# Performance work log

Hardware: AMD Instinct MI355X
Metric: run time of the kernel (lower is better)

The kernel has to match this reference:

```python
import jax, jax.numpy as jnp
import numpy as np

B, S, DIM = 1, 2048, 2048
H = 16
Q_LORA, KV_LORA = 1536, 512
D_NOPE, D_ROPE, D_V = 128, 64, 128
D_QK = D_NOPE + D_ROPE  # 192
EPS = 1e-6


def rms_norm(x, w, eps=EPS):
    var = jnp.mean(jnp.square(x), axis=-1, keepdims=True)
    return x * jax.lax.rsqrt(var + eps) * w


def apply_rope(x, cos, sin):
    # x: [B,S,H,D] with interleaved complex pairs; cos/sin: [S,D//2]
    x1, x2 = x[..., 0::2], x[..., 1::2]
    c = cos[None, :, None, :]
    s = sin[None, :, None, :]
    o1 = x1 * c - x2 * s
    o2 = x1 * s + x2 * c
    return jnp.stack([o1, o2], axis=-1).reshape(x.shape)


def setup_inputs() -> dict:
    key = jax.random.key(0)
    ks = jax.random.split(key, 8)
    x = jax.random.normal(ks[0], (B, S, DIM), dtype=jnp.float32)
    # rotary tables (standard complex exponentials)
    inv_freq = 1.0 / (10000.0 ** (np.arange(0, D_ROPE, 2, dtype=np.float32) / D_ROPE))
    t = np.arange(S, dtype=np.float32)
    freqs = np.outer(t, inv_freq)  # [S, D_ROPE//2]
    freqs_cos = jnp.asarray(np.cos(freqs))
    freqs_sin = jnp.asarray(np.sin(freqs))
    sd = lambda fan_in: 1.0 / np.sqrt(fan_in)
    wq_a = jax.random.normal(ks[1], (Q_LORA, DIM), dtype=jnp.float32) * sd(DIM)
    q_a_ln_w = jnp.ones((Q_LORA,), dtype=jnp.float32)
    wq_b = jax.random.normal(ks[2], (H * D_QK, Q_LORA), dtype=jnp.float32) * sd(Q_LORA)
    wkv_a = jax.random.normal(ks[3], (KV_LORA + D_ROPE, DIM), dtype=jnp.float32) * sd(DIM)
    kv_a_ln_w = jnp.ones((KV_LORA,), dtype=jnp.float32)
    wkv_b = jax.random.normal(ks[4], (H * (D_NOPE + D_V), KV_LORA), dtype=jnp.float32) * sd(KV_LORA)
    wo = jax.random.normal(ks[5], (DIM, H * D_V), dtype=jnp.float32) * sd(H * D_V)
    return {"x": x, "freqs_cos": freqs_cos, "freqs_sin": freqs_sin,
            "wq_a": wq_a, "q_a_ln_w": q_a_ln_w, "wq_b": wq_b,
            "wkv_a": wkv_a, "kv_a_ln_w": kv_a_ln_w, "wkv_b": wkv_b, "wo": wo}


def reference(x, freqs_cos, freqs_sin, wq_a, q_a_ln_w, wq_b, wkv_a, kv_a_ln_w, wkv_b, wo):
    softmax_scale = D_QK ** -0.5
    # Query: low-rank down-proj -> RMSNorm -> up-proj
    q = rms_norm(x @ wq_a.T, q_a_ln_w) @ wq_b.T            # [B,S,H*D_QK]
    q = q.reshape(B, S, H, D_QK)
    q_nope, q_pe = q[..., :D_NOPE], q[..., D_NOPE:]
    q_pe = apply_rope(q_pe, freqs_cos, freqs_sin)
    # KV: shared low-rank latent + decoupled rope key (MQA-style, 1 head)
    kv = x @ wkv_a.T                                        # [B,S,KV_LORA+D_ROPE]
    kv_c = rms_norm(kv[..., :KV_LORA], kv_a_ln_w)           # [B,S,KV_LORA]
    k_pe = apply_rope(kv[..., None, KV_LORA:], freqs_cos, freqs_sin)  # [B,S,1,D_ROPE]
    kvb = (kv_c @ wkv_b.T).reshape(B, S, H, D_NOPE + D_V)
    k_nope, v = kvb[..., :D_NOPE], kvb[..., D_NOPE:]
    # Attention scores: nope part + shared rope part
    scores = (jnp.einsum('bqhd,bkhd->bhqk', q_nope, k_nope)
              + jnp.einsum('bqhd,bkd->bhqk', q_pe, k_pe[:, :, 0, :])) * softmax_scale
    causal = jnp.tril(jnp.ones((S, S), dtype=bool))
    scores = jnp.where(causal[None, None], scores, -jnp.inf)
    p = jax.nn.softmax(scores, axis=-1)
    out = jnp.einsum('bhqk,bkhd->bqhd', p, v).reshape(B, S, H * D_V)
    return out @ wo.T
```

## Files before the change

kernel.cpp:

```cpp
#include <hip/hip_runtime.h>
#include <cstdint>
#include <cstddef>

typedef __bf16 bf16;
typedef bf16 bf16x8 __attribute__((ext_vector_type(8)));
typedef bf16 bf16x4 __attribute__((ext_vector_type(4)));
typedef float f32x4 __attribute__((ext_vector_type(4)));

typedef __attribute__((address_space(1))) void as1_void;
typedef __attribute__((address_space(3))) void as3_void;

#define INF __builtin_inff()

__global__ __launch_bounds__(256) void z100_cast_all(
    const float* __restrict__ x, const float* __restrict__ wq_a,
    const float* __restrict__ wkv_a, const float* __restrict__ wq_b,
    const float* __restrict__ wkv_b, const float* __restrict__ wo,
    bf16* __restrict__ x_bf, bf16* __restrict__ wab_bf,
    bf16* __restrict__ wqb_bf, bf16* __restrict__ wkvb_bf,
    bf16* __restrict__ wo_bf) {
    int i = blockIdx.x * 256 + threadIdx.x;
    const float* s;
    bf16* d;
    if (i < 1048576)      { s = x + (size_t)i * 4;                     d = x_bf + (size_t)i * 4; }
    else if (i < 1835008) { int o = i - 1048576; s = wq_a  + (size_t)o * 4; d = wab_bf + (size_t)o * 4; }
    else if (i < 2129920) { int o = i - 1835008; s = wkv_a + (size_t)o * 4; d = wab_bf + 1536ull * 2048 + (size_t)o * 4; }
    else if (i < 3309568) { int o = i - 2129920; s = wq_b  + (size_t)o * 4; d = wqb_bf + (size_t)o * 4; }
    else if (i < 3833856) { int o = i - 3309568; s = wkv_b + (size_t)o * 4; d = wkvb_bf + (size_t)o * 4; }
    else if (i < 4882432) { int o = i - 3833856; s = wo    + (size_t)o * 4; d = wo_bf + (size_t)o * 4; }
    else {                  int o = i - 4882432; bf16x4 z = {};
                            *(bf16x4*)(wab_bf + 2112ull * 2048 + (size_t)o * 4) = z; return; }
    float4 v = *(const float4*)s;
    bf16x4 ovec = { (bf16)v.x, (bf16)v.y, (bf16)v.z, (bf16)v.w };
    *(bf16x4*)d = ovec;
}

__global__ __launch_bounds__(256) void z100_rmsnorm(
    const float* __restrict__ x, int ldx, const float* __restrict__ w,
    bf16* __restrict__ y, int N, float invN) {
    const int row = blockIdx.x;
    const float* xr = x + (size_t)row * ldx;
    float ss = 0.f;
    for (int i = threadIdx.x * 4; i < N; i += 1024) {
        float4 v = *(const float4*)(xr + i);
        ss += v.x * v.x + v.y * v.y + v.z * v.z + v.w * v.w;
    }
    #pragma unroll
    for (int d = 1; d < 64; d <<= 1) ss += __shfl_xor(ss, d);
    __shared__ float red[4];
    if ((threadIdx.x & 63) == 0) red[threadIdx.x >> 6] = ss;
    __syncthreads();
    float tot = red[0] + red[1] + red[2] + red[3];
    float rs = rsqrtf(tot * invN + 1e-6f);
    bf16* yr = y + (size_t)row * N;
    for (int i = threadIdx.x * 4; i < N; i += 1024) {
        float4 v = *(const float4*)(xr + i);
        float4 wv = *(const float4*)(w + i);
        bf16x4 o = { (bf16)(v.x * rs * wv.x), (bf16)(v.y * rs * wv.y),
                     (bf16)(v.z * rs * wv.z), (bf16)(v.w * rs * wv.w) };
        *(bf16x4*)(yr + i) = o;
    }
}

__device__ __forceinline__ void gemm8_body(
    const bf16* __restrict__ A, const bf16* __restrict__ B,
    float* __restrict__ C, int N, int K, int ldc, int mblk, int nblk,
    bf16* AsB, bf16* BsB) {
    const int tid = threadIdx.x;
    const int lane = tid & 63, wave = tid >> 6;
    const int l15 = lane & 15, l4 = lane >> 4;
    const int m0 = mblk * 128, n0 = nblk * 128;
    const int wr = (wave >> 1) * 32, wc = (wave & 1) * 64;

    f32x4 acc[2][4] = {};

    const int srow = lane >> 2;
    const int scol = (lane & 3) * 8;
    const size_t a_base = (size_t)(m0 + wave * 16 + srow) * K + scol;
    const size_t b_base = (size_t)(n0 + wave * 16 + srow) * K + scol;

    auto stg = [&](int buf, int k0) {
        __builtin_amdgcn_global_load_lds((as1_void*)(void*)(A + a_base + k0),
                                         (as3_void*)(AsB + buf * 4096 + wave * 512), 16, 0, 0);
        __builtin_amdgcn_global_load_lds((as1_void*)(void*)(B + b_base + k0),
                                         (as3_void*)(BsB + buf * 4096 + wave * 512), 16, 0, 0);
    };

    const int nt = K >> 5;
    stg(0, 0);
    stg(1, 32);
    asm volatile("s_waitcnt vmcnt(2)" ::: "memory");
    __builtin_amdgcn_s_barrier();

    int cb = 0, sb = 2;
    for (int t = 0; t < nt; ++t) {
        if (t + 2 < nt) stg(sb, (t + 2) * 32);
        const bf16* Ab = AsB + cb * 4096;
        const bf16* Bb = BsB + cb * 4096;
        bf16x8 fa[2], fb[4];
        #pragma unroll
        for (int i = 0; i < 2; ++i)
            fa[i] = *(const bf16x8*)(Ab + (wr + 16 * i + l15) * 32 + 8 * l4);
        #pragma unroll
        for (int j = 0; j < 4; ++j)
            fb[j] = *(const bf16x8*)(Bb + (wc + 16 * j + l15) * 32 + 8 * l4);
        #pragma unroll
        for (int i = 0; i < 2; ++i)
            #pragma unroll
            for (int j = 0; j < 4; ++j)
                acc[i][j] = __builtin_amdgcn_mfma_f32_16x16x32_bf16(fa[i], fb[j], acc[i][j], 0, 0, 0);
        if (t + 2 < nt) { asm volatile("s_waitcnt vmcnt(2)" ::: "memory"); }
        else            { asm volatile("s_waitcnt vmcnt(0)" ::: "memory"); }
        __builtin_amdgcn_s_barrier();
        cb = (cb == 2) ? 0 : cb + 1;
        sb = (sb == 2) ? 0 : sb + 1;
    }

    #pragma unroll
    for (int i = 0; i < 2; ++i) {
        int row0 = m0 + wr + 16 * i + 4 * l4;
        #pragma unroll
        for (int j = 0; j < 4; ++j) {
            int col = n0 + wc + 16 * j + l15;
            if (col < N) {
                #pragma unroll
                for (int jj = 0; jj < 4; ++jj)
                    C[(size_t)(row0 + jj) * ldc + col] = acc[i][j][jj];
            }
        }
    }
}

__global__ __launch_bounds__(512) void z100_gemm8(
    const bf16* __restrict__ A, const bf16* __restrict__ B,
    float* __restrict__ C, int N, int K, int ldc) {
    __shared__ alignas(16) bf16 As[3 * 128 * 32];
    __shared__ alignas(16) bf16 Bs[3 * 128 * 32];
    gemm8_body(A, B, C, N, K, ldc, blockIdx.y, blockIdx.x, As, Bs);
}

__global__ __launch_bounds__(512) void z100_gemm_qkv(
    const bf16* __restrict__ qan, const bf16* __restrict__ wqb, float* __restrict__ qf,
    const bf16* __restrict__ kvc, const bf16* __restrict__ wkvb, float* __restrict__ kvbf) {
    __shared__ alignas(16) bf16 As[3 * 128 * 32];
    __shared__ alignas(16) bf16 Bs[3 * 128 * 32];
    const int bid = blockIdx.x;
    if (bid < 384) gemm8_body(qan, wqb, qf, 3072, 1536, 3072, bid / 24, bid % 24, As, Bs);
    else { int b = bid - 384; gemm8_body(kvc, wkvb, kvbf, 4096, 512, 4096, b / 32, b % 32, As, Bs); }
}

__global__ void z100_qk_prep(const float* __restrict__ q,
                             const float* __restrict__ kvb, const float* __restrict__ kpe,
                             int kpe_ld,
                             const float* __restrict__ fc, const float* __restrict__ fs,
                             bf16* __restrict__ q_attn, bf16* __restrict__ k_attn) {
    const int TOT = 2048 * 16 * 96;
    int u = blockIdx.x * 256 + threadIdx.x;
    if (u < TOT) {
        int e = u % 96;
        int sh = u / 96;
        int h = sh % 16, s = sh / 16;
        const float scale = 0.072168783649f;
        const float* qp = q + (size_t)s * 3072 + h * 192;
        bf16* o = q_attn + ((size_t)h * 2048 + s) * 192;
        if (e < 64) {
            o[2 * e]     = (bf16)(qp[2 * e] * scale);
            o[2 * e + 1] = (bf16)(qp[2 * e + 1] * scale);
        } else {
            int i = e - 64;
            float c = fc[s * 32 + i], sn = fs[s * 32 + i];
            float x1 = qp[128 + 2 * i], x2 = qp[128 + 2 * i + 1];
            o[128 + 2 * i]     = (bf16)((x1 * c - x2 * sn) * scale);
            o[128 + 2 * i + 1] = (bf16)((x1 * sn + x2 * c) * scale);
        }
    } else {
        u -= TOT;
        int e = u % 96;
        int sh = u / 96;
        int h = sh % 16, s = sh / 16;
        bf16* o = k_attn + ((size_t)h * 2048 + s) * 192;
        if (e < 64) {
            const float* kp = kvb + (size_t)s * 4096 + h * 256;
            o[2 * e]     = (bf16)kp[2 * e];
            o[2 * e + 1] = (bf16)kp[2 * e + 1];
        } else {
            int i = e - 64;
            float c = fc[s * 32 + i], sn = fs[s * 32 + i];
            float x1 = kpe[(size_t)s * kpe_ld + 2 * i];
            float x2 = kpe[(size_t)s * kpe_ld + 2 * i + 1];
            o[128 + 2 * i]     = (bf16)(x1 * c - x2 * sn);
            o[128 + 2 * i + 1] = (bf16)(x1 * sn + x2 * c);
        }
    }
}

__global__ __launch_bounds__(256) void z100_v_trans(const float* __restrict__ kvb,
                                                    bf16* __restrict__ vt) {
    const int st = blockIdx.x, h = blockIdx.y;
    const int s0 = st * 64;
    __shared__ alignas(16) bf16 tile[64 * 132];
    const int tid = threadIdx.x;
    #pragma unroll
    for (int i = 0; i < 8; ++i) {
        int slot = i * 256 + tid;
        int r = slot >> 5, c4 = slot & 31;
        float4 v = *(const float4*)(kvb + (size_t)(s0 + r) * 4096 + h * 256 + 128 + c4 * 4);
        bf16x4 o = { (bf16)v.x, (bf16)v.y, (bf16)v.z, (bf16)v.w };
        *(bf16x4*)(tile + r * 132 + c4 * 4) = o;
    }
    __syncthreads();
    #pragma unroll
    for (int i = 0; i < 4; ++i) {
        int slot = i * 256 + tid;
        int d = slot >> 3, ch = slot & 7;
        bf16x8 o;
        #pragma unroll
        for (int j = 0; j < 8; ++j) o[j] = tile[(ch * 8 + j) * 132 + d];
        *(bf16x8*)(vt + ((size_t)h * 128 + d) * 2048 + s0 + ch * 8) = o;
    }
}

__global__ __launch_bounds__(512) void z100_attn(
    const bf16* __restrict__ q_attn, const bf16* __restrict__ k_attn,
    const bf16* __restrict__ v_t, bf16* __restrict__ opart, float* __restrict__ ml) {
    const int bid = blockIdx.x;
    const int wk = (bid & 7) * 80 + (bid >> 3);
    const int h = wk / 40;
    const int s0w = wk - h * 40;
    int qt = 0, rem = s0w;
    while (rem >= (qt >> 2) + 1) { rem -= (qt >> 2) + 1; ++qt; }
    const int chk = rem;
    const int q0 = qt * 128;
    const int kstart = chk * 512;
    const int kend = min(q0 + 128, kstart + 512);
    const int slot = h * 40 + s0w;

    const int tid = threadIdx.x;
    const int lane = tid & 63, wave = tid >> 6;
    const int l15 = lane & 15, l4 = lane >> 4;

    __shared__ alignas(16) bf16 Ks[2][64 * 192];
    __shared__ alignas(16) bf16 Vs[2][128 * 64];

    const bf16* Qh = q_attn + (size_t)h * 2048 * 192;
    const bf16* Kh = k_attn + (size_t)h * 2048 * 192;
    const bf16* Vh = v_t + (size_t)h * 128 * 2048;

    const int wrow_max = q0 + wave * 16 + 15;
    const int diag_k0 = q0 + (wave >> 2) * 64;

    bf16x8 qf[6];
    {
        const bf16* qr = Qh + (size_t)(q0 + wave * 16 + l15) * 192 + 8 * l4;
        #pragma unroll
        for (int c = 0; c < 6; ++c) qf[c] = *(const bf16x8*)(qr + 32 * c);
    }

    int koff[3], voff[2];
    #pragma unroll
    for (int i = 0; i < 3; ++i) {
        int off = (wave * 3 + i) * 1024 + lane * 16;
        int r = off / 384;
        int ch = (off % 384) >> 4;
        int ksrc = (r & 0x23) | ((r & 0x0C) << 1) | ((r & 0x10) >> 2);
        koff[i] = ksrc * 192 + (ch ^ (r & 7)) * 8;
    }
    #pragma unroll
    for (int i = 0; i < 2; ++i) {
        int off = (wave * 2 + i) * 1024 + lane * 16;
        int d = off >> 7;
        int ch = (off >> 4) & 7;
        voff[i] = d * 2048 + (ch ^ (d & 7)) * 8;
    }

    auto stage = [&](int buf, int k0) {
        #pragma unroll
        for (int i = 0; i < 3; ++i)
            __builtin_amdgcn_global_load_lds(
                (as1_void*)(void*)(Kh + (size_t)k0 * 192 + koff[i]),
                (as3_void*)((char*)&Ks[buf][0] + (wave * 3 + i) * 1024), 16, 0, 0);
        #pragma unroll
        for (int i = 0; i < 2; ++i)
            __builtin_amdgcn_global_load_lds(
                (as1_void*)(void*)(Vh + k0 + voff[i]),
                (as3_void*)((char*)&Vs[buf][0] + (wave * 2 + i) * 1024), 16, 0, 0);
    };

    f32x4 oacc[8] = {};
    float m_r = -INF, l_r = 0.f;
    const int nt = (kend - kstart) >> 6;

    stage(0, kstart);
    __syncthreads();
    int cur = 0;
    for (int t = 0; t < nt; ++t) {
        const int k0 = kstart + t * 64;
        if (t + 1 < nt) stage(cur ^ 1, k0 + 64);

        if (k0 <= wrow_max) {
            const char* KsC = (const char*)&Ks[cur][0];
            const char* VsC = (const char*)&Vs[cur][0];

            f32x4 sc[4];
            __builtin_amdgcn_s_setprio(1);
            #pragma unroll
            for (int kt = 0; kt < 4; ++kt) {
                f32x4 a = { 0.f, 0.f, 0.f, 0.f };
                int r = 16 * kt + l15;
                #pragma unroll
                for (int c = 0; c < 6; ++c) {
                    int byteo = (r * 384 + c * 64 + l4 * 16) ^ ((r & 7) << 4);
                    bf16x8 kf = *(const bf16x8*)(KsC + byteo);
                    a = __builtin_amdgcn_mfma_f32_16x16x32_bf16(kf, qf[c], a, 0, 0, 0);
                }
                sc[kt] = a;
            }
            __builtin_amdgcn_s_setprio(0);

            if (k0 == diag_k0) {
                int qrow = (wave & 3) * 16 + l15;
                #pragma unroll
                for (int kt = 0; kt < 4; ++kt)
                    #pragma unroll
                    for (int r = 0; r < 4; ++r) {
                        int kl = ((kt >> 1) << 5) | (l4 << 3) | ((kt & 1) << 2) | r;
                        if (kl > qrow) sc[kt][r] = -INF;
                    }
            }

            float mx = -INF;
            #pragma unroll
            for (int kt = 0; kt < 4; ++kt)
                #pragma unroll
                for (int r = 0; r < 4; ++r) mx = fmaxf(mx, sc[kt][r]);
            mx = fmaxf(mx, __shfl_xor(mx, 16));
            mx = fmaxf(mx, __shfl_xor(mx, 32));
            float mnew = fmaxf(m_r, mx);
            float corr = __expf(m_r - mnew);
            float rs = 0.f;
            #pragma unroll
            for (int kt = 0; kt < 4; ++kt)
                #pragma unroll
                for (int r = 0; r < 4; ++r) {
                    float pv = __expf(sc[kt][r] - mnew);
                    sc[kt][r] = pv;
                    rs += pv;
                }
            rs += __shfl_xor(rs, 16);
            rs += __shfl_xor(rs, 32);
            l_r = l_r * corr + rs;
            m_r = mnew;

            float c_r[4];
            #pragma unroll
            for (int r = 0; r < 4; ++r) c_r[r] = __shfl(corr, 20 * l4 + r);
            #pragma unroll
            for (int dt = 0; dt < 8; ++dt)
                #pragma unroll
                for (int r = 0; r < 4; ++r) oacc[dt][r] *= c_r[r];

            bf16x8 pf[2];
            #pragma unroll
            for (int c2 = 0; c2 < 2; ++c2)
                #pragma unroll
                for (int i = 0; i < 8; ++i)
                    pf[c2][i] = (bf16)sc[2 * c2 + (i >> 2)][i & 3];

            __builtin_amdgcn_s_setprio(1);
            #pragma unroll
            for (int dt = 0; dt < 8; ++dt) {
                #pragma unroll
                for (int c2 = 0; c2 < 2; ++c2) {
                    int d = 16 * dt + l15;
                    int byteo = (d * 128 + c2 * 64 + l4 * 16) ^ ((d & 7) << 4);
                    bf16x8 vf = *(const bf16x8*)(VsC + byteo);
                    oacc[dt] = __builtin_amdgcn_mfma_f32_16x16x32_bf16(pf[c2], vf, oacc[dt], 0, 0, 0);
                }
            }
            __builtin_amdgcn_s_setprio(0);
        }

        __syncthreads();
        cur ^= 1;
    }

    const int qr_base = wave * 16;
    if (lane < 16) {
        ml[(size_t)slot * 256 + qr_base + lane] = m_r;
        ml[(size_t)slot * 256 + 128 + qr_base + lane] = l_r;
    }
    bf16* ob = opart + (size_t)slot * 16384;
    #pragma unroll
    for (int dt = 0; dt < 8; ++dt) {
        int d = 16 * dt + l15;
        #pragma unroll
        for (int r = 0; r < 4; ++r) {
            int qr = qr_base + 4 * l4 + r;
            ob[qr * 128 + d] = (bf16)oacc[dt][r];
        }
    }
}

__global__ __launch_bounds__(256) void z100_attn_combine(
    const bf16* __restrict__ opart, const float* __restrict__ ml, bf16* __restrict__ ao) {
    const int qt = blockIdx.x, h = blockIdx.y;
    const int t = threadIdx.x;
    const int qr = t >> 1, d0 = (t & 1) * 64;
    const int np = (qt >> 2) + 1;
    int base = 0;
    for (int j = 0; j < qt; ++j) base += (j >> 2) + 1;
    const int slot0 = h * 40 + base;
    float m[4], l[4], w[4];
    float M = -INF;
    #pragma unroll
    for (int i = 0; i < 4; ++i)
        if (i < np) {
            m[i] = ml[(size_t)(slot0 + i) * 256 + qr];
            l[i] = ml[(size_t)(slot0 + i) * 256 + 128 + qr];
            M = fmaxf(M, m[i]);
        }
    float L = 0.f;
    #pragma unroll
    for (int i = 0; i < 4; ++i)
        if (i < np) {
            w[i] = __expf(m[i] - M);
            L += w[i] * l[i];
        }
    float invL = 1.f / L;
    bf16* orow = ao + (size_t)(qt * 128 + qr) * 2048 + h * 128 + d0;
    for (int d = 0; d < 64; d += 8) {
        float acc[8] = {};
        #pragma unroll
        for (int i = 0; i < 4; ++i)
            if (i < np) {
                bf16x8 a = *(const bf16x8*)(opart + (size_t)(slot0 + i) * 16384 + qr * 128 + d0 + d);
                #pragma unroll
                for (int j = 0; j < 8; ++j) acc[j] += w[i] * (float)a[j];
            }
        bf16x8 o;
        #pragma unroll
        for (int j = 0; j < 8; ++j) o[j] = (bf16)(acc[j] * invL);
        *(bf16x8*)(orow + d) = o;
    }
}

extern "C" void kernel_launch(void* const* d_in, const int* in_sizes, int n_in,
                              void* d_out, int out_size, void* d_ws, size_t ws_size,
                              hipStream_t stream) {
    (void)in_sizes; (void)n_in; (void)out_size; (void)ws_size;
    const float* x     = (const float*)d_in[0];
    const float* fc    = (const float*)d_in[1];
    const float* fs    = (const float*)d_in[2];
    const float* wq_a  = (const float*)d_in[3];
    const float* q_ln  = (const float*)d_in[4];
    const float* wq_b  = (const float*)d_in[5];
    const float* wkv_a = (const float*)d_in[6];
    const float* kv_ln = (const float*)d_in[7];
    const float* wkv_b = (const float*)d_in[8];
    const float* wo    = (const float*)d_in[9];
    float* out = (float*)d_out;

    char* p = (char*)d_ws;
    auto alloc = [&](size_t bytes) {
        char* r = p;
        p += (bytes + 255) & ~(size_t)255;
        return r;
    };
    char* phase1  = p;
    bf16* x_bf    = (bf16*)alloc(2048ull * 2048 * 2);
    bf16* wab_bf  = (bf16*)alloc(2176ull * 2048 * 2);
    float* qa_f   = (float*)alloc(2048ull * 2112 * 4);
    bf16* qan_bf  = (bf16*)alloc(2048ull * 1536 * 2);
    bf16* wqb_bf  = (bf16*)alloc(3072ull * 1536 * 2);
    bf16* wkvb_bf = (bf16*)alloc(4096ull * 512 * 2);
    bf16* wo_bf   = (bf16*)alloc(2048ull * 2048 * 2);
    float* q_f    = (float*)alloc(2048ull * 3072 * 4);
    bf16* kvc_bf  = (bf16*)alloc(2048ull * 512 * 2);
    float* kvb_f  = (float*)alloc(2048ull * 4096 * 4);
    bf16* q_attn  = (bf16*)alloc(16ull * 2048 * 192 * 2);
    bf16* k_attn  = (bf16*)alloc(16ull * 2048 * 192 * 2);
    bf16* v_t     = (bf16*)alloc(16ull * 128 * 2048 * 2);
    bf16* ao_bf   = (bf16*)alloc(2048ull * 2048 * 2);
    bf16* opart   = (bf16*)phase1;
    float* mlbuf  = (float*)(phase1 + 640ull * 16384 * 2);

    z100_cast_all<<<19200, 256, 0, stream>>>(x, wq_a, wkv_a, wq_b, wkv_b, wo,
                                             x_bf, wab_bf, wqb_bf, wkvb_bf, wo_bf);

    z100_gemm8<<<dim3(17, 16), 512, 0, stream>>>(x_bf, wab_bf, qa_f, 2112, 2048, 2112);
    z100_rmsnorm<<<2048, 256, 0, stream>>>(qa_f, 2112, q_ln, qan_bf, 1536, 1.f / 1536.f);
    z100_rmsnorm<<<2048, 256, 0, stream>>>(qa_f + 1536, 2112, kv_ln, kvc_bf, 512, 1.f / 512.f);

    z100_gemm_qkv<<<dim3(896), 512, 0, stream>>>(qan_bf, wqb_bf, q_f, kvc_bf, wkvb_bf, kvb_f);

    z100_qk_prep<<<24576, 256, 0, stream>>>(q_f, kvb_f, qa_f + 2048, 2112, fc, fs, q_attn, k_attn);
    z100_v_trans<<<dim3(32, 16), 256, 0, stream>>>(kvb_f, v_t);

    z100_attn<<<dim3(640), 512, 0, stream>>>(q_attn, k_attn, v_t, opart, mlbuf);
    z100_attn_combine<<<dim3(16, 16), 256, 0, stream>>>(opart, mlbuf, ao_bf);

    z100_gemm8<<<dim3(16, 16), 512, 0, stream>>>(ao_bf, wo_bf, out, 2048, 2048, 2048);
}
```

Measured before the change: 244.1 us.

## Enlarge attention query tile to 256 rows with two row-groups per wave

The split-K attention kernel now processes 256 query rows per block (32 per wave, as two 16-row MFMA groups) over fixed 256-key chunks instead of 128 rows over 512-key chunks. Each K/V tile staged in LDS is reused by twice as many query rows, which cuts redundant K/V loads. The combine kernel is reworked for up to 8 partials per 256-row tile. In exchange each wave holds twice the accumulator registers, which may lower occupancy. Diagonal tiles also waste some MFMA work on zero probabilities for the inactive group, and there are fewer blocks (576) to balance across CUs.

```diff
diff --git a/kernel.cpp b/kernel.cpp
--- a/kernel.cpp
+++ b/kernel.cpp
@@ -224,16 +224,15 @@
     const bf16* __restrict__ q_attn, const bf16* __restrict__ k_attn,
     const bf16* __restrict__ v_t, bf16* __restrict__ opart, float* __restrict__ ml) {
     const int bid = blockIdx.x;
-    const int wk = (bid & 7) * 80 + (bid >> 3);
-    const int h = wk / 40;
-    const int s0w = wk - h * 40;
+    const int wk = (bid & 7) * 72 + (bid >> 3);
+    const int h = wk / 36;
+    const int s0w = wk - h * 36;
     int qt = 0, rem = s0w;
-    while (rem >= (qt >> 2) + 1) { rem -= (qt >> 2) + 1; ++qt; }
+    while (rem >= qt + 1) { rem -= qt + 1; ++qt; }
     const int chk = rem;
-    const int q0 = qt * 128;
-    const int kstart = chk * 512;
-    const int kend = min(q0 + 128, kstart + 512);
-    const int slot = h * 40 + s0w;
+    const int q0 = qt * 256;
+    const int kstart = chk * 256;
+    const int slot = h * 36 + s0w;
 
     const int tid = threadIdx.x;
     const int lane = tid & 63, wave = tid >> 6;
@@ -246,14 +245,14 @@
     const bf16* Kh = k_attn + (size_t)h * 2048 * 192;
     const bf16* Vh = v_t + (size_t)h * 128 * 2048;
 
-    const int wrow_max = q0 + wave * 16 + 15;
-    const int diag_k0 = q0 + (wave >> 2) * 64;
-
-    bf16x8 qf[6];
-    {
-        const bf16* qr = Qh + (size_t)(q0 + wave * 16 + l15) * 192 + 8 * l4;
-        #pragma unroll
-        for (int c = 0; c < 6; ++c) qf[c] = *(const bf16x8*)(qr + 32 * c);
+    const int wq0 = q0 + wave * 32;
+
+    bf16x8 qf[2][6];
+    #pragma unroll
+    for (int g = 0; g < 2; ++g) {
+        const bf16* qr = Qh + (size_t)(wq0 + g * 16 + l15) * 192 + 8 * l4;
+        #pragma unroll
+        for (int c = 0; c < 6; ++c) qf[g][c] = *(const bf16x8*)(qr + 32 * c);
     }
 
     int koff[3], voff[2];
@@ -286,85 +285,105 @@
                 (as3_void*)((char*)&Vs[buf][0] + (wave * 2 + i) * 1024), 16, 0, 0);
     };
 
-    f32x4 oacc[8] = {};
-    float m_r = -INF, l_r = 0.f;
-    const int nt = (kend - kstart) >> 6;
+    f32x4 oacc0[8] = {}, oacc1[8] = {};
+    float m_r0 = -INF, m_r1 = -INF, l_r0 = 0.f, l_r1 = 0.f;
+
+    auto softmax_g = [&](float& mr, float& lr, f32x4 (&oac)[8],
+                         f32x4 (&scg)[4], bf16x8 (&pfg)[2]) {
+        float mx = -INF;
+        #pragma unroll
+        for (int kt = 0; kt < 4; ++kt)
+            #pragma unroll
+            for (int r = 0; r < 4; ++r) mx = fmaxf(mx, scg[kt][r]);
+        mx = fmaxf(mx, __shfl_xor(mx, 16));
+        mx = fmaxf(mx, __shfl_xor(mx, 32));
+        float mnew = fmaxf(mr, mx);
+        float corr = __expf(mr - mnew);
+        float rs = 0.f;
+        #pragma unroll
+        for (int kt = 0; kt < 4; ++kt)
+            #pragma unroll
+            for (int r = 0; r < 4; ++r) {
+                float pv = __expf(scg[kt][r] - mnew);
+                scg[kt][r] = pv;
+                rs += pv;
+            }
+        rs += __shfl_xor(rs, 16);
+        rs += __shfl_xor(rs, 32);
+        lr = lr * corr + rs;
+        mr = mnew;
+        float c_r[4];
+        #pragma unroll
+        for (int r = 0; r < 4; ++r) c_r[r] = __shfl(corr, 20 * l4 + r);
+        #pragma unroll
+        for (int dt = 0; dt < 8; ++dt)
+            #pragma unroll
+            for (int r = 0; r < 4; ++r) oac[dt][r] *= c_r[r];
+        #pragma unroll
+        for (int c2 = 0; c2 < 2; ++c2)
+            #pragma unroll
+            for (int i = 0; i < 8; ++i)
+                pfg[c2][i] = (bf16)scg[2 * c2 + (i >> 2)][i & 3];
+    };
 
     stage(0, kstart);
     __syncthreads();
     int cur = 0;
-    for (int t = 0; t < nt; ++t) {
+    #pragma unroll 1
+    for (int t = 0; t < 4; ++t) {
         const int k0 = kstart + t * 64;
-        if (t + 1 < nt) stage(cur ^ 1, k0 + 64);
-
-        if (k0 <= wrow_max) {
+        if (t + 1 < 4) stage(cur ^ 1, k0 + 64);
+
+        const bool act1 = (k0 <= wq0 + 31);
+        const bool act0 = (k0 <= wq0 + 15);
+        if (act1) {
             const char* KsC = (const char*)&Ks[cur][0];
             const char* VsC = (const char*)&Vs[cur][0];
 
-            f32x4 sc[4];
+            f32x4 sc[2][4];
             __builtin_amdgcn_s_setprio(1);
             #pragma unroll
             for (int kt = 0; kt < 4; ++kt) {
-                f32x4 a = { 0.f, 0.f, 0.f, 0.f };
+                f32x4 a0 = { 0.f, 0.f, 0.f, 0.f };
+                f32x4 a1 = { 0.f, 0.f, 0.f, 0.f };
                 int r = 16 * kt + l15;
                 #pragma unroll
                 for (int c = 0; c < 6; ++c) {
                     int byteo = (r * 384 + c * 64 + l4 * 16) ^ ((r & 7) << 4);
                     bf16x8 kf = *(const bf16x8*)(KsC + byteo);
-                    a = __builtin_amdgcn_mfma_f32_16x16x32_bf16(kf, qf[c], a, 0, 0, 0);
+                    a0 = __builtin_amdgcn_mfma_f32_16x16x32_bf16(kf, qf[0][c], a0, 0, 0, 0);
+                    a1 = __builtin_amdgcn_mfma_f32_16x16x32_bf16(kf, qf[1][c], a1, 0, 0, 0);
                 }
-                sc[kt] = a;
+                sc[0][kt] = a0;
+                sc[1][kt] = a1;
             }
             __builtin_amdgcn_s_setprio(0);
 
-            if (k0 == diag_k0) {
-                int qrow = (wave & 3) * 16 + l15;
+            #pragma unroll
+            for (int g = 0; g < 2; ++g) {
+                int gidx = (wave << 1) + g;
+                if (k0 == q0 + (gidx >> 2) * 64) {
+                    int qrow = (gidx & 3) * 16 + l15;
+                    #pragma unroll
+                    for (int kt = 0; kt < 4; ++kt)
+                        #pragma unroll
+                        for (int r = 0; r < 4; ++r) {
+                            int kl = ((kt >> 1) << 5) | (l4 << 3) | ((kt & 1) << 2) | r;
+                            if (kl > qrow) sc[g][kt][r] = -INF;
+                        }
+                }
+            }
+
+            bf16x8 pf0[2], pf1[2];
+            softmax_g(m_r1, l_r1, oacc1, sc[1], pf1);
+            if (act0) {
+                softmax_g(m_r0, l_r0, oacc0, sc[0], pf0);
+            } else {
                 #pragma unroll
-                for (int kt = 0; kt < 4; ++kt)
+                for (int c2 = 0; c2 < 2; ++c2)
                     #pragma unroll
-                    for (int r = 0; r < 4; ++r) {
-                        int kl = ((kt >> 1) << 5) | (l4 << 3) | ((kt & 1) << 2) | r;
-                        if (kl > qrow) sc[kt][r] = -INF;
-                    }
-            }
-
-            float mx = -INF;
-            #pragma unroll
-            for (int kt = 0; kt < 4; ++kt)
-                #pragma unroll
-                for (int r = 0; r < 4; ++r) mx = fmaxf(mx, sc[kt][r]);
-            mx = fmaxf(mx, __shfl_xor(mx, 16));
-            mx = fmaxf(mx, __shfl_xor(mx, 32));
-            float mnew = fmaxf(m_r, mx);
-            float corr = __expf(m_r - mnew);
-            float rs = 0.f;
-            #pragma unroll
-            for (int kt = 0; kt < 4; ++kt)
-                #pragma unroll
-                for (int r = 0; r < 4; ++r) {
-                    float pv = __expf(sc[kt][r] - mnew);
-                    sc[kt][r] = pv;
-                    rs += pv;
-                }
-            rs += __shfl_xor(rs, 16);
-            rs += __shfl_xor(rs, 32);
-            l_r = l_r * corr + rs;
-            m_r = mnew;
-
-            float c_r[4];
-            #pragma unroll
-            for (int r = 0; r < 4; ++r) c_r[r] = __shfl(corr, 20 * l4 + r);
-            #pragma unroll
-            for (int dt = 0; dt < 8; ++dt)
-                #pragma unroll
-                for (int r = 0; r < 4; ++r) oacc[dt][r] *= c_r[r];
-
-            bf16x8 pf[2];
-            #pragma unroll
-            for (int c2 = 0; c2 < 2; ++c2)
-                #pragma unroll
-                for (int i = 0; i < 8; ++i)
-                    pf[c2][i] = (bf16)sc[2 * c2 + (i >> 2)][i & 3];
+                    for (int i = 0; i < 8; ++i) pf0[c2][i] = (bf16)0.f;
+            }
 
             __builtin_amdgcn_s_setprio(1);
             #pragma unroll
@@ -374,7 +393,8 @@
                     int d = 16 * dt + l15;
                     int byteo = (d * 128 + c2 * 64 + l4 * 16) ^ ((d & 7) << 4);
                     bf16x8 vf = *(const bf16x8*)(VsC + byteo);
-                    oacc[dt] = __builtin_amdgcn_mfma_f32_16x16x32_bf16(pf[c2], vf, oacc[dt], 0, 0, 0);
+                    oacc1[dt] = __builtin_amdgcn_mfma_f32_16x16x32_bf16(pf1[c2], vf, oacc1[dt], 0, 0, 0);
+                    oacc0[dt] = __builtin_amdgcn_mfma_f32_16x16x32_bf16(pf0[c2], vf, oacc0[dt], 0, 0, 0);
                 }
             }
             __builtin_amdgcn_s_setprio(0);
@@ -384,56 +404,57 @@
         cur ^= 1;
     }
 
-    const int qr_base = wave * 16;
     if (lane < 16) {
-        ml[(size_t)slot * 256 + qr_base + lane] = m_r;
-        ml[(size_t)slot * 256 + 128 + qr_base + lane] = l_r;
-    }
-    bf16* ob = opart + (size_t)slot * 16384;
+        ml[(size_t)slot * 512 + wave * 32 + lane] = m_r0;
+        ml[(size_t)slot * 512 + wave * 32 + 16 + lane] = m_r1;
+        ml[(size_t)slot * 512 + 256 + wave * 32 + lane] = l_r0;
+        ml[(size_t)slot * 512 + 256 + wave * 32 + 16 + lane] = l_r1;
+    }
+    bf16* ob = opart + (size_t)slot * 32768;
     #pragma unroll
     for (int dt = 0; dt < 8; ++dt) {
         int d = 16 * dt + l15;
         #pragma unroll
         for (int r = 0; r < 4; ++r) {
-            int qr = qr_base + 4 * l4 + r;
-            ob[qr * 128 + d] = (bf16)oacc[dt][r];
-        }
-    }
-}
-
-__global__ __launch_bounds__(256) void z100_attn_combine(
+            int qr0 = wave * 32 + 4 * l4 + r;
+            ob[qr0 * 128 + d] = (bf16)oacc0[dt][r];
+            ob[(qr0 + 16) * 128 + d] = (bf16)oacc1[dt][r];
+        }
+    }
+}
+
+__global__ __launch_bounds__(512) void z100_attn_combine(
     const bf16* __restrict__ opart, const float* __restrict__ ml, bf16* __restrict__ ao) {
     const int qt = blockIdx.x, h = blockIdx.y;
     const int t = threadIdx.x;
     const int qr = t >> 1, d0 = (t & 1) * 64;
-    const int np = (qt >> 2) + 1;
-    int base = 0;
-    for (int j = 0; j < qt; ++j) base += (j >> 2) + 1;
-    const int slot0 = h * 40 + base;
-    float m[4], l[4], w[4];
+    const int np = qt + 1;
+    const int base = qt * (qt + 1) / 2;
+    const int slot0 = h * 36 + base;
+    float m[8], l[8], w[8];
     float M = -INF;
     #pragma unroll
-    for (int i = 0; i < 4; ++i)
+    for (int i = 0; i < 8; ++i)
         if (i < np) {
-            m[i] = ml[(size_t)(slot0 + i) * 256 + qr];
-            l[i] = ml[(size_t)(slot0 + i) * 256 + 128 + qr];
+            m[i] = ml[(size_t)(slot0 + i) * 512 + qr];
+            l[i] = ml[(size_t)(slot0 + i) * 512 + 256 + qr];
             M = fmaxf(M, m[i]);
         }
     float L = 0.f;
     #pragma unroll
-    for (int i = 0; i < 4; ++i)
+    for (int i = 0; i < 8; ++i)
         if (i < np) {
             w[i] = __expf(m[i] - M);
             L += w[i] * l[i];
         }
     float invL = 1.f / L;
-    bf16* orow = ao + (size_t)(qt * 128 + qr) * 2048 + h * 128 + d0;
+    bf16* orow = ao + (size_t)(qt * 256 + qr) * 2048 + h * 128 + d0;
     for (int d = 0; d < 64; d += 8) {
         float acc[8] = {};
         #pragma unroll
-        for (int i = 0; i < 4; ++i)
+        for (int i = 0; i < 8; ++i)
             if (i < np) {
-                bf16x8 a = *(const bf16x8*)(opart + (size_t)(slot0 + i) * 16384 + qr * 128 + d0 + d);
+                bf16x8 a = *(const bf16x8*)(opart + (size_t)(slot0 + i) * 32768 + qr * 128 + d0 + d);
                 #pragma unroll
                 for (int j = 0; j < 8; ++j) acc[j] += w[i] * (float)a[j];
             }
@@ -482,7 +503,7 @@
     bf16* v_t     = (bf16*)alloc(16ull * 128 * 2048 * 2);
     bf16* ao_bf   = (bf16*)alloc(2048ull * 2048 * 2);
     bf16* opart   = (bf16*)phase1;
-    float* mlbuf  = (float*)(phase1 + 640ull * 16384 * 2);
+    float* mlbuf  = (float*)(phase1 + 576ull * 32768 * 2);
 
     z100_cast_all<<<19200, 256, 0, stream>>>(x, wq_a, wkv_a, wq_b, wkv_b, wo,
                                              x_bf, wab_bf, wqb_bf, wkvb_bf, wo_bf);
@@ -496,8 +517,8 @@
     z100_qk_prep<<<24576, 256, 0, stream>>>(q_f, kvb_f, qa_f + 2048, 2112, fc, fs, q_attn, k_attn);
     z100_v_trans<<<dim3(32, 16), 256, 0, stream>>>(kvb_f, v_t);
 
-    z100_attn<<<dim3(640), 512, 0, stream>>>(q_attn, k_attn, v_t, opart, mlbuf);
-    z100_attn_combine<<<dim3(16, 16), 256, 0, stream>>>(opart, mlbuf, ao_bf);
+    z100_attn<<<dim3(576), 512, 0, stream>>>(q_attn, k_attn, v_t, opart, mlbuf);
+    z100_attn_combine<<<dim3(8, 16), 512, 0, stream>>>(opart, mlbuf, ao_bf);
 
     z100_gemm8<<<dim3(16, 16), 512, 0, stream>>>(ao_bf, wo_bf, out, 2048, 2048, 2048);
 }
```

Result: slower. 298.6 us (+22.3%).

## Use 4-wave GEMM blocks with 64x64 warp tiles and coalesced attention combine

Applied to the files above, without the earlier changes.

The shared GEMM body moves from 8 waves with 32x64 per-wave tiles to 4 waves with 64x64 per-wave tiles on the same 128x128 block tile. Each wave now issues two LDS-direct loads per operand per stage, and the vmcnt waits are adjusted to match. This raises MFMA work per LDS fragment load and cuts the per-block wave count, at the cost of more accumulator registers per wave. The attention combine kernel is also reworked to use 512 threads striding over 8-element chunks so that reads and writes are contiguous across lanes.

```diff
diff --git a/kernel.cpp b/kernel.cpp
--- a/kernel.cpp
+++ b/kernel.cpp
@@ -62,7 +62,7 @@
     }
 }
 
-__device__ __forceinline__ void gemm8_body(
+__device__ __forceinline__ void gemm4_body(
     const bf16* __restrict__ A, const bf16* __restrict__ B,
     float* __restrict__ C, int N, int K, int ldc, int mblk, int nblk,
     bf16* AsB, bf16* BsB) {
@@ -70,26 +70,32 @@
     const int lane = tid & 63, wave = tid >> 6;
     const int l15 = lane & 15, l4 = lane >> 4;
     const int m0 = mblk * 128, n0 = nblk * 128;
-    const int wr = (wave >> 1) * 32, wc = (wave & 1) * 64;
-
-    f32x4 acc[2][4] = {};
+    const int wr = (wave >> 1) * 64, wc = (wave & 1) * 64;
+
+    f32x4 acc[4][4] = {};
 
     const int srow = lane >> 2;
     const int scol = (lane & 3) * 8;
-    const size_t a_base = (size_t)(m0 + wave * 16 + srow) * K + scol;
-    const size_t b_base = (size_t)(n0 + wave * 16 + srow) * K + scol;
+    const size_t a_base = (size_t)(m0 + wave * 32 + srow) * K + scol;
+    const size_t b_base = (size_t)(n0 + wave * 32 + srow) * K + scol;
 
     auto stg = [&](int buf, int k0) {
+        bf16* AsW = AsB + buf * 4096 + wave * 1024;
+        bf16* BsW = BsB + buf * 4096 + wave * 1024;
         __builtin_amdgcn_global_load_lds((as1_void*)(void*)(A + a_base + k0),
-                                         (as3_void*)(AsB + buf * 4096 + wave * 512), 16, 0, 0);
+                                         (as3_void*)AsW, 16, 0, 0);
+        __builtin_amdgcn_global_load_lds((as1_void*)(void*)(A + a_base + (size_t)16 * K + k0),
+                                         (as3_void*)(AsW + 512), 16, 0, 0);
         __builtin_amdgcn_global_load_lds((as1_void*)(void*)(B + b_base + k0),
-                                         (as3_void*)(BsB + buf * 4096 + wave * 512), 16, 0, 0);
+                                         (as3_void*)BsW, 16, 0, 0);
+        __builtin_amdgcn_global_load_lds((as1_void*)(void*)(B + b_base + (size_t)16 * K + k0),
+                                         (as3_void*)(BsW + 512), 16, 0, 0);
     };
 
     const int nt = K >> 5;
     stg(0, 0);
     stg(1, 32);
-    asm volatile("s_waitcnt vmcnt(2)" ::: "memory");
+    asm volatile("s_waitcnt vmcnt(4)" ::: "memory");
     __builtin_amdgcn_s_barrier();
 
     int cb = 0, sb = 2;
@@ -97,19 +103,19 @@
         if (t + 2 < nt) stg(sb, (t + 2) * 32);
         const bf16* Ab = AsB + cb * 4096;
         const bf16* Bb = BsB + cb * 4096;
-        bf16x8 fa[2], fb[4];
-        #pragma unroll
-        for (int i = 0; i < 2; ++i)
+        bf16x8 fa[4], fb[4];
+        #pragma unroll
+        for (int i = 0; i < 4; ++i)
             fa[i] = *(const bf16x8*)(Ab + (wr + 16 * i + l15) * 32 + 8 * l4);
         #pragma unroll
         for (int j = 0; j < 4; ++j)
             fb[j] = *(const bf16x8*)(Bb + (wc + 16 * j + l15) * 32 + 8 * l4);
         #pragma unroll
-        for (int i = 0; i < 2; ++i)
+        for (int i = 0; i < 4; ++i)
             #pragma unroll
             for (int j = 0; j < 4; ++j)
                 acc[i][j] = __builtin_amdgcn_mfma_f32_16x16x32_bf16(fa[i], fb[j], acc[i][j], 0, 0, 0);
-        if (t + 2 < nt) { asm volatile("s_waitcnt vmcnt(2)" ::: "memory"); }
+        if (t + 2 < nt) { asm volatile("s_waitcnt vmcnt(4)" ::: "memory"); }
         else            { asm volatile("s_waitcnt vmcnt(0)" ::: "memory"); }
         __builtin_amdgcn_s_barrier();
         cb = (cb == 2) ? 0 : cb + 1;
@@ -117,7 +123,7 @@
     }
 
     #pragma unroll
-    for (int i = 0; i < 2; ++i) {
+    for (int i = 0; i < 4; ++i) {
         int row0 = m0 + wr + 16 * i + 4 * l4;
         #pragma unroll
         for (int j = 0; j < 4; ++j) {
@@ -131,22 +137,22 @@
     }
 }
 
-__global__ __launch_bounds__(512) void z100_gemm8(
+__global__ __launch_bounds__(256) void z100_gemm4(
     const bf16* __restrict__ A, const bf16* __restrict__ B,
     float* __restrict__ C, int N, int K, int ldc) {
     __shared__ alignas(16) bf16 As[3 * 128 * 32];
     __shared__ alignas(16) bf16 Bs[3 * 128 * 32];
-    gemm8_body(A, B, C, N, K, ldc, blockIdx.y, blockIdx.x, As, Bs);
-}
-
-__global__ __launch_bounds__(512) void z100_gemm_qkv(
+    gemm4_body(A, B, C, N, K, ldc, blockIdx.y, blockIdx.x, As, Bs);
+}
+
+__global__ __launch_bounds__(256) void z100_gemm_qkv(
     const bf16* __restrict__ qan, const bf16* __restrict__ wqb, float* __restrict__ qf,
     const bf16* __restrict__ kvc, const bf16* __restrict__ wkvb, float* __restrict__ kvbf) {
     __shared__ alignas(16) bf16 As[3 * 128 * 32];
     __shared__ alignas(16) bf16 Bs[3 * 128 * 32];
     const int bid = blockIdx.x;
-    if (bid < 384) gemm8_body(qan, wqb, qf, 3072, 1536, 3072, bid / 24, bid % 24, As, Bs);
-    else { int b = bid - 384; gemm8_body(kvc, wkvb, kvbf, 4096, 512, 4096, b / 32, b % 32, As, Bs); }
+    if (bid < 384) gemm4_body(qan, wqb, qf, 3072, 1536, 3072, bid / 24, bid % 24, As, Bs);
+    else { int b = bid - 384; gemm4_body(kvc, wkvb, kvbf, 4096, 512, 4096, b / 32, b % 32, As, Bs); }
 }
 
 __global__ void z100_qk_prep(const float* __restrict__ q,
@@ -401,46 +407,48 @@
     }
 }
 
-__global__ __launch_bounds__(256) void z100_attn_combine(
+__global__ __launch_bounds__(512) void z100_attn_combine(
     const bf16* __restrict__ opart, const float* __restrict__ ml, bf16* __restrict__ ao) {
     const int qt = blockIdx.x, h = blockIdx.y;
     const int t = threadIdx.x;
-    const int qr = t >> 1, d0 = (t & 1) * 64;
     const int np = (qt >> 2) + 1;
     int base = 0;
     for (int j = 0; j < qt; ++j) base += (j >> 2) + 1;
     const int slot0 = h * 40 + base;
-    float m[4], l[4], w[4];
-    float M = -INF;
-    #pragma unroll
-    for (int i = 0; i < 4; ++i)
-        if (i < np) {
-            m[i] = ml[(size_t)(slot0 + i) * 256 + qr];
-            l[i] = ml[(size_t)(slot0 + i) * 256 + 128 + qr];
-            M = fmaxf(M, m[i]);
-        }
-    float L = 0.f;
-    #pragma unroll
-    for (int i = 0; i < 4; ++i)
-        if (i < np) {
-            w[i] = __expf(m[i] - M);
-            L += w[i] * l[i];
-        }
-    float invL = 1.f / L;
-    bf16* orow = ao + (size_t)(qt * 128 + qr) * 2048 + h * 128 + d0;
-    for (int d = 0; d < 64; d += 8) {
-        float acc[8] = {};
+    #pragma unroll 1
+    for (int it = 0; it < 4; ++it) {
+        const int c = it * 512 + t;
+        const int qr = c >> 4;
+        const int dc = (c & 15) * 8;
+        float m[4], l[4], w[4];
+        float M = -INF;
         #pragma unroll
         for (int i = 0; i < 4; ++i)
             if (i < np) {
-                bf16x8 a = *(const bf16x8*)(opart + (size_t)(slot0 + i) * 16384 + qr * 128 + d0 + d);
+                m[i] = ml[(size_t)(slot0 + i) * 256 + qr];
+                l[i] = ml[(size_t)(slot0 + i) * 256 + 128 + qr];
+                M = fmaxf(M, m[i]);
+            }
+        float L = 0.f;
+        #pragma unroll
+        for (int i = 0; i < 4; ++i)
+            if (i < np) {
+                w[i] = __expf(m[i] - M);
+                L += w[i] * l[i];
+            }
+        float invL = 1.f / L;
+        float acc[8] = {};
+        #pragma unroll
+        for (int i = 0; i < 4; ++i)
+            if (i < np) {
+                bf16x8 a = *(const bf16x8*)(opart + (size_t)(slot0 + i) * 16384 + (size_t)c * 8);
                 #pragma unroll
                 for (int j = 0; j < 8; ++j) acc[j] += w[i] * (float)a[j];
             }
         bf16x8 o;
         #pragma unroll
         for (int j = 0; j < 8; ++j) o[j] = (bf16)(acc[j] * invL);
-        *(bf16x8*)(orow + d) = o;
+        *(bf16x8*)(ao + (size_t)(qt * 128 + qr) * 2048 + h * 128 + dc) = o;
     }
 }
 
@@ -487,17 +495,17 @@
     z100_cast_all<<<19200, 256, 0, stream>>>(x, wq_a, wkv_a, wq_b, wkv_b, wo,
                                              x_bf, wab_bf, wqb_bf, wkvb_bf, wo_bf);
 
-    z100_gemm8<<<dim3(17, 16), 512, 0, stream>>>(x_bf, wab_bf, qa_f, 2112, 2048, 2112);
+    z100_gemm4<<<dim3(17, 16), 256, 0, stream>>>(x_bf, wab_bf, qa_f, 2112, 2048, 2112);
     z100_rmsnorm<<<2048, 256, 0, stream>>>(qa_f, 2112, q_ln, qan_bf, 1536, 1.f / 1536.f);
     z100_rmsnorm<<<2048, 256, 0, stream>>>(qa_f + 1536, 2112, kv_ln, kvc_bf, 512, 1.f / 512.f);
 
-    z100_gemm_qkv<<<dim3(896), 512, 0, stream>>>(qan_bf, wqb_bf, q_f, kvc_bf, wkvb_bf, kvb_f);
+    z100_gemm_qkv<<<dim3(896), 256, 0, stream>>>(qan_bf, wqb_bf, q_f, kvc_bf, wkvb_bf, kvb_f);
 
     z100_qk_prep<<<24576, 256, 0, stream>>>(q_f, kvb_f, qa_f + 2048, 2112, fc, fs, q_attn, k_attn);
     z100_v_trans<<<dim3(32, 16), 256, 0, stream>>>(kvb_f, v_t);
 
     z100_attn<<<dim3(640), 512, 0, stream>>>(q_attn, k_attn, v_t, opart, mlbuf);
-    z100_attn_combine<<<dim3(16, 16), 256, 0, stream>>>(opart, mlbuf, ao_bf);
-
-    z100_gemm8<<<dim3(16, 16), 512, 0, stream>>>(ao_bf, wo_bf, out, 2048, 2048, 2048);
-}
+    z100_attn_combine<<<dim3(16, 16), 512, 0, stream>>>(opart, mlbuf, ao_bf);
+
+    z100_gemm4<<<dim3(16, 16), 256, 0, stream>>>(ao_bf, wo_bf, out, 2048, 2048, 2048);
+}
```

Result: slower. 258.5 us (+5.9%).
